# Optimization experiments

Hardware: AMD Instinct MI355X
Metric: run time of the kernel (lower is better)

The kernel has to match this reference:

```python
import jax, jax.numpy as jnp
import numpy as np

N_HEADS = 16
N_KV_HEADS = 4
WINDOW = 128
THETA = 10000.0


def _rope_cos_sin(T, half):
    inv = 1.0 / (THETA ** (jnp.arange(half, dtype=jnp.float32) / half))
    f = jnp.arange(T, dtype=jnp.float32)[:, None] * inv[None, :]  # (T, half)
    return jnp.cos(f), jnp.sin(f)


def _apply_rope(x, cos, sin):
    # x: (B, H, T, hd); interleaved (real, imag) pairs like torch view_as_complex
    xr, xi = x[..., 0::2], x[..., 1::2]
    out_r = xr * cos - xi * sin
    out_i = xr * sin + xi * cos
    return jnp.stack([out_r, out_i], axis=-1).reshape(x.shape)


def setup_inputs() -> dict:
    key = jax.random.key(0)
    ks = jax.random.split(key, 6)
    B, T, C = 1, 4096, 2048
    kvC = (C // N_HEADS) * N_KV_HEADS
    return {
        "x": jax.random.normal(ks[0], (B, T, C), dtype=jnp.float32),
        "wq": jax.random.normal(ks[1], (C, C), dtype=jnp.float32) * 0.02,
        "wk": jax.random.normal(ks[2], (C, kvC), dtype=jnp.float32) * 0.02,
        "wv": jax.random.normal(ks[3], (C, kvC), dtype=jnp.float32) * 0.02,
        "wo": jax.random.normal(ks[4], (C, C), dtype=jnp.float32) * 0.02,
        "sink": jnp.zeros((1, N_HEADS, 1, 1), dtype=jnp.float32),
    }


def reference(x, wq, wk, wv, wo, sink):
    B, T, C = x.shape
    hd = C // N_HEADS
    n_rep = N_HEADS // N_KV_HEADS

    q = (x @ wq).reshape(B, T, N_HEADS, hd).transpose(0, 2, 1, 3)    # (B,H,T,hd)
    k = (x @ wk).reshape(B, T, N_KV_HEADS, hd).transpose(0, 2, 1, 3)  # (B,Hkv,T,hd)
    v = (x @ wv).reshape(B, T, N_KV_HEADS, hd).transpose(0, 2, 1, 3)

    cos, sin = _rope_cos_sin(T, hd // 2)  # (T, hd/2), broadcasts over (B,H,T,hd/2)
    q = _apply_rope(q, cos, sin)
    k = _apply_rope(k, cos, sin)

    # GQA head expansion (repeat_interleave over head dim)
    k = jnp.repeat(k, n_rep, axis=1)
    v = jnp.repeat(v, n_rep, axis=1)

    att = jnp.einsum("bhqd,bhkd->bhqk", q, k) * (hd ** -0.5) + sink

    # symmetric sliding-window band: |i - j| <= window//2
    idx = jnp.arange(T)
    band = jnp.abs(idx[:, None] - idx[None, :]) <= (WINDOW // 2)
    att = jnp.where(band[None, None, :, :], att, -jnp.inf)

    att = jax.nn.softmax(att, axis=-1)
    # torch code replaces NaN rows (fully-masked) with uniform; band always has diag so no-op
    att = jnp.where(jnp.isnan(att), 1.0 / T, att)

    out = jnp.einsum("bhqk,bhkd->bqhd", att, v).reshape(B, T, C)
    return out @ wo
```

## Files before the change

kernel.cpp:

```cpp
#include <hip/hip_runtime.h>
#include <stdint.h>

#define T_SEQ 4096
#define C_DIM 2048
#define HD 128

typedef unsigned short ushort_t;
typedef __attribute__((ext_vector_type(8))) short shortx8;
typedef __attribute__((ext_vector_type(4))) float floatx4;
typedef __attribute__((ext_vector_type(8))) unsigned short u16x8;
typedef __attribute__((ext_vector_type(4))) unsigned short u16x4;

__device__ __forceinline__ ushort_t f2bf(float f) {
  union { float f; uint32_t u; } v; v.f = f;
  v.u += 0x7fffu + ((v.u >> 16) & 1u);
  return (ushort_t)(v.u >> 16);
}
__device__ __forceinline__ void load_lds16(const ushort_t* g, ushort_t* l) {
  __builtin_amdgcn_global_load_lds(
      (const __attribute__((address_space(1))) unsigned int*)g,
      (__attribute__((address_space(3))) unsigned int*)l, 16, 0, 0);
}

__global__ __launch_bounds__(256) void prep_kernel(
    const float* __restrict__ wq, const float* __restrict__ wk,
    const float* __restrict__ wv, const float* __restrict__ wo,
    const float* __restrict__ x,
    ushort_t* __restrict__ BtAll, ushort_t* __restrict__ woT,
    ushort_t* __restrict__ xb) {
  const int bid = blockIdx.x;
  const int tid = threadIdx.x;
  if (bid >= 2560) {
    int i = (bid - 2560) * 256 + tid;
    float4 v = ((const float4*)x)[i];
    u16x4 o; o[0] = f2bf(v.x); o[1] = f2bf(v.y); o[2] = f2bf(v.z); o[3] = f2bf(v.w);
    ((u16x4*)xb)[i] = o;
    return;
  }
  const float* src; ushort_t* dst; int C, bx, by;
  if (bid < 1024) { src = wq; dst = BtAll; C = 2048; bx = bid & 31; by = bid >> 5; }
  else if (bid < 1280) { int b = bid - 1024; src = wk; dst = BtAll + (size_t)2048 * 2048; C = 512; bx = b & 7; by = b >> 3; }
  else if (bid < 1536) { int b = bid - 1280; src = wv; dst = BtAll + (size_t)2560 * 2048; C = 512; bx = b & 7; by = b >> 3; }
  else { int b = bid - 1536; src = wo; dst = woT; C = 2048; bx = b & 31; by = b >> 5; }
  const int R = 2048;

  __shared__ float tile[64][65];
  const int c0 = bx * 64, r0 = by * 64;
  for (int i = tid; i < 1024; i += 256) {
    int r = i >> 4, cc = (i & 15) * 4;
    float4 v = *(const float4*)&src[(size_t)(r0 + r) * C + c0 + cc];
    tile[r][cc] = v.x; tile[r][cc + 1] = v.y; tile[r][cc + 2] = v.z; tile[r][cc + 3] = v.w;
  }
  __syncthreads();
  for (int i = tid; i < 512; i += 256) {
    int oc = i >> 3;
    int g = (i & 7) * 8;
    u16x8 o;
    for (int j = 0; j < 8; ++j) o[j] = f2bf(tile[g + j][oc]);
    *(u16x8*)&dst[(size_t)(c0 + oc) * R + r0 + g] = o;
  }
}

struct GemmAcc { floatx4 a[4][4]; };

__device__ __forceinline__ void gemm_core_bk64(
    const ushort_t* __restrict__ A, const ushort_t* __restrict__ Bt,
    ushort_t* As, ushort_t* Bs, GemmAcc& acc,
    int m0, int n0, int K, int tid, int lane, int wave, int quad, int l16,
    int wm, int wn) {
  const int nk = K >> 6;
  for (int kk = 0; kk < nk; ++kk) {
    const int k0 = kk << 6;
    for (int r = 0; r < 4; ++r) {
      int e = r * 256 + tid;
      int row = e >> 3;
      int p = e & 7;
      int g = (p - row) & 7;
      const ushort_t* ga = A + (size_t)(m0 + row) * K + k0 + g * 8;
      const ushort_t* gb = Bt + (size_t)(n0 + row) * K + k0 + g * 8;
      ushort_t* la = As + (size_t)(r * 256 + (tid & 192)) * 8;
      ushort_t* lb = Bs + (size_t)(r * 256 + (tid & 192)) * 8;
      load_lds16(ga, la);
      load_lds16(gb, lb);
    }
    __syncthreads();
    for (int ks = 0; ks < 2; ++ks) {
      shortx8 af[4], bfr[4];
      for (int i = 0; i < 4; ++i) {
        int ar = wm + i * 16 + l16;
        af[i] = *(const shortx8*)(As + ar * 64 + (((ks << 2) + quad + ar) & 7) * 8);
        int br = wn + i * 16 + l16;
        bfr[i] = *(const shortx8*)(Bs + br * 64 + (((ks << 2) + quad + br) & 7) * 8);
      }
      for (int i = 0; i < 4; ++i)
        for (int j = 0; j < 4; ++j)
          acc.a[i][j] = __builtin_amdgcn_mfma_f32_16x16x32_bf16(af[i], bfr[j], acc.a[i][j], 0, 0, 0);
    }
    __syncthreads();
  }
}

__global__ __launch_bounds__(256, 3) void gemm_qkv(
    const ushort_t* __restrict__ A, const ushort_t* __restrict__ Bt,
    ushort_t* __restrict__ qbb, ushort_t* __restrict__ kbb,
    ushort_t* __restrict__ vtb) {
  __shared__ __align__(16) ushort_t As[128 * 64];
  __shared__ __align__(16) ushort_t Bs[128 * 64];
  const int tid = threadIdx.x;
  const int lane = tid & 63;
  const int wave = tid >> 6;
  const int quad = lane >> 4;
  const int l16 = lane & 15;
  const int m0 = blockIdx.y * 128;
  const int n0 = blockIdx.x * 128;
  const int wm = (wave & 1) * 64;
  const int wn = (wave >> 1) * 64;

  GemmAcc acc = {};
  gemm_core_bk64(A, Bt, As, Bs, acc, m0, n0, 2048, tid, lane, wave, quad, l16, wm, wn);

  if (blockIdx.x < 20) {
    const bool isq = (blockIdx.x < 16);
    const int par = l16 & 1;
    for (int j = 0; j < 4; ++j) {
      int col = n0 + wn + j * 16 + l16;
      int irot = (col & 127) >> 1;
      float inv = __expf(-0.14391157f * (float)irot);
      for (int i = 0; i < 4; ++i) {
        int t0r = m0 + wm + i * 16 + quad * 4;
        for (int r = 0; r < 4; ++r) {
          float val = acc.a[i][j][r];
          float other = __shfl_xor(val, 1, 64);
          float sn, cs;
          __sincosf((float)(t0r + r) * inv, &sn, &cs);
          float outv = par ? (other * sn + val * cs) : (val * cs - other * sn);
          if (isq) qbb[(size_t)(t0r + r) * 2048 + col] = f2bf(outv);
          else     kbb[(size_t)(t0r + r) * 512 + (col - 2048)] = f2bf(outv);
        }
      }
    }
  } else {
    for (int j = 0; j < 4; ++j) {
      int dim = n0 + wn + j * 16 + l16 - 2560;
      for (int i = 0; i < 4; ++i) {
        int t0r = m0 + wm + i * 16 + quad * 4;
        u16x4 o;
        for (int r = 0; r < 4; ++r) o[r] = f2bf(acc.a[i][j][r]);
        *(u16x4*)&vtb[(size_t)dim * T_SEQ + t0r] = o;
      }
    }
  }
}

__global__ __launch_bounds__(256, 3) void gemm_bf16(
    const ushort_t* __restrict__ A, const ushort_t* __restrict__ Bt,
    float* __restrict__ C, int M, int N, int K) {
  __shared__ __align__(16) ushort_t As[128 * 64];
  __shared__ __align__(16) ushort_t Bs[128 * 64];
  const int tid = threadIdx.x;
  const int lane = tid & 63;
  const int wave = tid >> 6;
  const int quad = lane >> 4;
  const int l16 = lane & 15;
  const int m0 = blockIdx.y * 128;
  const int n0 = blockIdx.x * 128;
  const int wm = (wave & 1) * 64;
  const int wn = (wave >> 1) * 64;

  GemmAcc acc = {};
  gemm_core_bk64(A, Bt, As, Bs, acc, m0, n0, K, tid, lane, wave, quad, l16, wm, wn);

  for (int i = 0; i < 4; ++i)
    for (int j = 0; j < 4; ++j) {
      int col = n0 + wn + j * 16 + l16;
      int rbase = m0 + wm + i * 16 + quad * 4;
      for (int r = 0; r < 4; ++r)
        C[(size_t)(rbase + r) * N + col] = acc.a[i][j][r];
    }
}

#define LSTR 168
__global__ __launch_bounds__(256, 2) void attn_kernel(
    const ushort_t* __restrict__ qbb, const ushort_t* __restrict__ kbb,
    const ushort_t* __restrict__ vtb, ushort_t* __restrict__ ao) {
  __shared__ __align__(16) ushort_t QP[64 * LSTR];
  __shared__ __align__(16) ushort_t KV[160 * LSTR];

  const int tid = threadIdx.x;
  const int lane = tid & 63;
  const int wave = tid >> 6;
  const int l16 = lane & 15;
  const int quad = lane >> 4;
  const int h0 = blockIdx.x * 2;
  const int kvh = h0 >> 2;
  const int t0 = blockIdx.y * 32;
  const int kstart = t0 - 64;
  const int hsel = wave & 1;
  const int qh = wave >> 1;
  const float scale = 0.08838834764831845f;

  for (int c = tid; c < 1024; c += 256) {
    int row = c >> 4, c8 = c & 15;
    int h = h0 + (row >> 5);
    int q = t0 + (row & 31);
    u16x8 v = *(const u16x8*)&qbb[(size_t)q * C_DIM + h * HD + c8 * 8];
    *(u16x8*)&QP[row * LSTR + c8 * 8] = v;
  }
  for (int c = tid; c < 2560; c += 256) {
    int row = c >> 4, c8 = c & 15;
    int t = kstart + row;
    u16x8 v;
    if (t >= 0 && t < T_SEQ) {
      v = *(const u16x8*)&kbb[(size_t)t * 512 + kvh * HD + c8 * 8];
    } else {
      for (int z = 0; z < 8; ++z) v[z] = 0;
    }
    *(u16x8*)&KV[row * LSTR + c8 * 8] = v;
  }
  __syncthreads();

  floatx4 acc[10] = {};
  const int arow = hsel * 32 + qh * 16 + l16;
  for (int ks = 0; ks < 4; ++ks) {
    shortx8 af = *(const shortx8*)&QP[arow * LSTR + ks * 32 + quad * 8];
    for (int kt = 0; kt < 10; ++kt) {
      shortx8 bf = *(const shortx8*)&KV[(kt * 16 + l16) * LSTR + ks * 32 + quad * 8];
      acc[kt] = __builtin_amdgcn_mfma_f32_16x16x32_bf16(af, bf, acc[kt], 0, 0, 0);
    }
  }

  float mrow[4] = {-3e38f, -3e38f, -3e38f, -3e38f};
  for (int kt = 0; kt < 10; ++kt) {
    int col = kt * 16 + l16;
    int kg = kstart + col;
    for (int r = 0; r < 4; ++r) {
      int row = qh * 16 + quad * 4 + r;
      bool valid = (kg >= 0) && (kg < T_SEQ) && (col >= row) && (col <= row + 128);
      float s = valid ? acc[kt][r] * scale : -3e38f;
      acc[kt][r] = s;
      mrow[r] = fmaxf(mrow[r], s);
    }
  }
  for (int off = 1; off < 16; off <<= 1)
    for (int r = 0; r < 4; ++r)
      mrow[r] = fmaxf(mrow[r], __shfl_xor(mrow[r], off, 64));
  float rl[4];
  for (int r = 0; r < 4; ++r) {
    float s = 0.f;
    for (int kt = 0; kt < 10; ++kt) {
      float p = expf(acc[kt][r] - mrow[r]);
      acc[kt][r] = p;
      s += p;
    }
    rl[r] = s;
  }
  for (int off = 1; off < 16; off <<= 1)
    for (int r = 0; r < 4; ++r) rl[r] += __shfl_xor(rl[r], off, 64);
  for (int r = 0; r < 4; ++r) rl[r] = 1.0f / rl[r];

  __syncthreads();

  for (int kt = 0; kt < 10; ++kt) {
    int col = kt * 16 + l16;
    for (int r = 0; r < 4; ++r) {
      int row = hsel * 32 + qh * 16 + quad * 4 + r;
      QP[row * LSTR + col] = f2bf(acc[kt][r] * rl[r]);
    }
  }
  for (int c = tid; c < 2560; c += 256) {
    int dim = c / 20, c8 = c % 20;
    int k0 = kstart + c8 * 8;
    const ushort_t* g = &vtb[(size_t)(kvh * HD + dim) * T_SEQ];
    u16x8 v;
    if (k0 >= 0 && k0 + 7 < T_SEQ) {
      v = *(const u16x8*)&g[k0];
    } else {
      for (int z = 0; z < 8; ++z) {
        int kk = k0 + z;
        v[z] = (kk >= 0 && kk < T_SEQ) ? g[kk] : (ushort_t)0;
      }
    }
    *(u16x8*)&KV[dim * LSTR + c8 * 8] = v;
  }
  __syncthreads();

  floatx4 oacc[8] = {};
  const int prow = hsel * 32 + qh * 16 + l16;
  for (int ks = 0; ks < 5; ++ks) {
    shortx8 pf = *(const shortx8*)&QP[prow * LSTR + ks * 32 + quad * 8];
    for (int dt = 0; dt < 8; ++dt) {
      shortx8 vf = *(const shortx8*)&KV[(dt * 16 + l16) * LSTR + ks * 32 + quad * 8];
      oacc[dt] = __builtin_amdgcn_mfma_f32_16x16x32_bf16(pf, vf, oacc[dt], 0, 0, 0);
    }
  }

  const int h = h0 + hsel;
  for (int r = 0; r < 4; ++r) {
    int row = t0 + qh * 16 + quad * 4 + r;
    for (int dt = 0; dt < 8; ++dt) {
      int dim = dt * 16 + l16;
      ao[(size_t)row * C_DIM + h * HD + dim] = f2bf(oacc[dt][r]);
    }
  }
}

extern "C" void kernel_launch(void* const* d_in, const int* in_sizes, int n_in,
                              void* d_out, int out_size, void* d_ws, size_t ws_size,
                              hipStream_t stream) {
  const float* x  = (const float*)d_in[0];
  const float* wq = (const float*)d_in[1];
  const float* wk = (const float*)d_in[2];
  const float* wv = (const float*)d_in[3];
  const float* wo = (const float*)d_in[4];
  float* out = (float*)d_out;

  char* ws = (char*)d_ws;
  ushort_t* BtAll = (ushort_t*)(ws);
  ushort_t* woT   = (ushort_t*)(ws + 12582912);
  ushort_t* xb    = (ushort_t*)(ws + 20971520);
  ushort_t* qbb   = (ushort_t*)(ws + 37748736);
  ushort_t* kbb   = (ushort_t*)(ws + 54525952);
  ushort_t* vtb   = (ushort_t*)(ws + 58720256);
  ushort_t* ao    = (ushort_t*)(ws + 62914560);

  prep_kernel<<<10752, 256, 0, stream>>>(wq, wk, wv, wo, x, BtAll, woT, xb);

  gemm_qkv<<<dim3(24, 32), 256, 0, stream>>>(xb, BtAll, qbb, kbb, vtb);

  attn_kernel<<<dim3(8, 128), 256, 0, stream>>>(qbb, kbb, vtb, ao);

  gemm_bf16<<<dim3(16, 32), 256, 0, stream>>>(ao, woT, out, 4096, 2048, 2048);
}
```

Measured before the change: 243.8 us.

## Replace QKV GEMM with 256x256 double-buffered 8-wave kernel and fast exp

The QKV projection GEMM is rewritten to use 256x256 output tiles with 512 threads. It double-buffers LDS, prefetches global-to-LDS loads interleaved with the MFMA phases, sets wave priority around the MFMAs, and applies a swizzled block order for L2 locality. The larger tiles give more data reuse per loaded byte and hide load latency, at the cost of more LDS and register pressure and only 192 blocks, which may leave the 256 CUs underfilled. Separately, the attention softmax switches from expf to __expf, which is cheaper but less precise.

```diff
diff --git a/kernel.cpp b/kernel.cpp
--- a/kernel.cpp
+++ b/kernel.cpp
@@ -100,58 +100,6 @@
   }
 }
 
-__global__ __launch_bounds__(256, 3) void gemm_qkv(
-    const ushort_t* __restrict__ A, const ushort_t* __restrict__ Bt,
-    ushort_t* __restrict__ qbb, ushort_t* __restrict__ kbb,
-    ushort_t* __restrict__ vtb) {
-  __shared__ __align__(16) ushort_t As[128 * 64];
-  __shared__ __align__(16) ushort_t Bs[128 * 64];
-  const int tid = threadIdx.x;
-  const int lane = tid & 63;
-  const int wave = tid >> 6;
-  const int quad = lane >> 4;
-  const int l16 = lane & 15;
-  const int m0 = blockIdx.y * 128;
-  const int n0 = blockIdx.x * 128;
-  const int wm = (wave & 1) * 64;
-  const int wn = (wave >> 1) * 64;
-
-  GemmAcc acc = {};
-  gemm_core_bk64(A, Bt, As, Bs, acc, m0, n0, 2048, tid, lane, wave, quad, l16, wm, wn);
-
-  if (blockIdx.x < 20) {
-    const bool isq = (blockIdx.x < 16);
-    const int par = l16 & 1;
-    for (int j = 0; j < 4; ++j) {
-      int col = n0 + wn + j * 16 + l16;
-      int irot = (col & 127) >> 1;
-      float inv = __expf(-0.14391157f * (float)irot);
-      for (int i = 0; i < 4; ++i) {
-        int t0r = m0 + wm + i * 16 + quad * 4;
-        for (int r = 0; r < 4; ++r) {
-          float val = acc.a[i][j][r];
-          float other = __shfl_xor(val, 1, 64);
-          float sn, cs;
-          __sincosf((float)(t0r + r) * inv, &sn, &cs);
-          float outv = par ? (other * sn + val * cs) : (val * cs - other * sn);
-          if (isq) qbb[(size_t)(t0r + r) * 2048 + col] = f2bf(outv);
-          else     kbb[(size_t)(t0r + r) * 512 + (col - 2048)] = f2bf(outv);
-        }
-      }
-    }
-  } else {
-    for (int j = 0; j < 4; ++j) {
-      int dim = n0 + wn + j * 16 + l16 - 2560;
-      for (int i = 0; i < 4; ++i) {
-        int t0r = m0 + wm + i * 16 + quad * 4;
-        u16x4 o;
-        for (int r = 0; r < 4; ++r) o[r] = f2bf(acc.a[i][j][r]);
-        *(u16x4*)&vtb[(size_t)dim * T_SEQ + t0r] = o;
-      }
-    }
-  }
-}
-
 __global__ __launch_bounds__(256, 3) void gemm_bf16(
     const ushort_t* __restrict__ A, const ushort_t* __restrict__ Bt,
     float* __restrict__ C, int M, int N, int K) {
@@ -179,6 +127,143 @@
     }
 }
 
+#define BARF() do { __builtin_amdgcn_s_barrier(); asm volatile("" ::: "memory"); } while (0)
+
+__global__ __launch_bounds__(512, 2) void gemm_qkv256(
+    const ushort_t* __restrict__ A, const ushort_t* __restrict__ Bt,
+    ushort_t* __restrict__ qbb, ushort_t* __restrict__ kbb,
+    ushort_t* __restrict__ vtb) {
+  __shared__ __align__(16) ushort_t SA[2][16384];
+  __shared__ __align__(16) ushort_t SB[2][16384];
+  const int tid = threadIdx.x;
+  const int lane = tid & 63;
+  const int w = tid >> 6;
+  const int l16 = lane & 15;
+  const int quad = lane >> 4;
+  const int wm = (w >> 2) * 128;
+  const int wn = (w & 3) * 64;
+  const int aq = wm + (w & 3) * 16;
+  const int bq = wn + (w >> 2) * 16;
+  const int gl8 = lane >> 3;
+  const int gch = ((lane & 7) - gl8) & 7;
+
+  const int bid = blockIdx.x;
+  const int swz = (bid & 7) * 24 + (bid >> 3);
+  const int n0 = (swz % 12) * 256;
+  const int m0 = (swz / 12) * 256;
+
+  const int off0 = l16 * 64 + ((quad + l16) & 7) * 8;
+  const int off1 = l16 * 64 + ((4 + quad + l16) & 7) * 8;
+
+  floatx4 acc[8][4] = {};
+
+  auto issue2 = [&](const ushort_t* __restrict__ G, int gRow, ushort_t* L, int r0, int k0) {
+#pragma unroll
+    for (int u = 0; u < 2; ++u) {
+      const ushort_t* src = G + (size_t)(gRow + r0 + u * 8 + gl8) * 2048 + k0 + gch * 8;
+      load_lds16(src, L + (r0 + u * 8) * 64);
+    }
+  };
+
+  issue2(A, m0, SA[0], aq, 0);        issue2(A, m0, SA[0], aq + 64, 0);
+  issue2(Bt, n0, SB[0], bq, 0);       issue2(Bt, n0, SB[0], bq + 32, 0);
+  issue2(A, m0, SA[1], aq, 64);       issue2(A, m0, SA[1], aq + 64, 64);
+  issue2(Bt, n0, SB[1], bq, 64);      issue2(Bt, n0, SB[1], bq + 32, 64);
+  asm volatile("s_waitcnt vmcnt(8)" ::: "memory");
+  BARF();
+
+  for (int t2 = 0; t2 < 16; ++t2) {
+#pragma unroll
+    for (int half = 0; half < 2; ++half) {
+      const int t = t2 * 2 + half;
+      const ushort_t* SAb = SA[half];
+      const ushort_t* SBb = SB[half];
+      ushort_t* SAo = SA[half ^ 1];
+      ushort_t* SBo = SB[half ^ 1];
+#pragma unroll
+      for (int p = 0; p < 4; ++p) {
+        const int ih = p >> 1, jh = p & 1;
+        shortx8 af0[4], af1[4], bf0[2], bf1[2];
+#pragma unroll
+        for (int i2 = 0; i2 < 4; ++i2) {
+          const int rb = (wm + (ih * 4 + i2) * 16) * 64;
+          af0[i2] = *(const shortx8*)&SAb[rb + off0];
+          af1[i2] = *(const shortx8*)&SAb[rb + off1];
+        }
+#pragma unroll
+        for (int j2 = 0; j2 < 2; ++j2) {
+          const int rb = (wn + (jh * 2 + j2) * 16) * 64;
+          bf0[j2] = *(const shortx8*)&SBb[rb + off0];
+          bf1[j2] = *(const shortx8*)&SBb[rb + off1];
+        }
+        if (p == 0)      { if (t > 0 && t + 1 < 32) issue2(A, m0, SAo, aq + 64, (t + 1) * 64); }
+        else if (p == 1) { if (t > 0 && t + 1 < 32) issue2(Bt, n0, SBo, bq + 32, (t + 1) * 64); }
+        else if (p == 2) { if (t + 2 < 32) issue2(A, m0, (ushort_t*)SAb, aq, (t + 2) * 64); }
+        else             { if (t + 2 < 32) issue2(Bt, n0, (ushort_t*)SBb, bq, (t + 2) * 64); }
+        BARF();
+        asm volatile("s_waitcnt lgkmcnt(0)" ::: "memory");
+        __builtin_amdgcn_s_setprio(1);
+#pragma unroll
+        for (int ks = 0; ks < 2; ++ks)
+#pragma unroll
+          for (int i2 = 0; i2 < 4; ++i2)
+#pragma unroll
+            for (int j2 = 0; j2 < 2; ++j2)
+              acc[ih * 4 + i2][jh * 2 + j2] = __builtin_amdgcn_mfma_f32_16x16x32_bf16(
+                  ks ? af1[i2] : af0[i2], ks ? bf1[j2] : bf0[j2],
+                  acc[ih * 4 + i2][jh * 2 + j2], 0, 0, 0);
+        __builtin_amdgcn_s_setprio(0);
+        if (p == 3) {
+          if (t < 30)       { asm volatile("s_waitcnt vmcnt(4)" ::: "memory"); }
+          else if (t == 30) { asm volatile("s_waitcnt vmcnt(0)" ::: "memory"); }
+        }
+        BARF();
+      }
+    }
+  }
+
+  asm volatile("s_waitcnt vmcnt(0) lgkmcnt(0)" ::: "memory");
+  BARF();
+
+  if (n0 < 2560) {
+    const bool isq = (n0 < 2048);
+    const int par = l16 & 1;
+#pragma unroll
+    for (int j = 0; j < 4; ++j) {
+      int col = n0 + wn + j * 16 + l16;
+      int irot = (col & 127) >> 1;
+      float inv = __expf(-0.14391157f * (float)irot);
+#pragma unroll
+      for (int i = 0; i < 8; ++i) {
+        int t0r = m0 + wm + i * 16 + quad * 4;
+#pragma unroll
+        for (int r = 0; r < 4; ++r) {
+          float val = acc[i][j][r];
+          float other = __shfl_xor(val, 1, 64);
+          float sn, cs;
+          __sincosf((float)(t0r + r) * inv, &sn, &cs);
+          float outv = par ? (other * sn + val * cs) : (val * cs - other * sn);
+          if (isq) qbb[(size_t)(t0r + r) * 2048 + col] = f2bf(outv);
+          else     kbb[(size_t)(t0r + r) * 512 + (col - 2048)] = f2bf(outv);
+        }
+      }
+    }
+  } else {
+#pragma unroll
+    for (int j = 0; j < 4; ++j) {
+      int dim = n0 + wn + j * 16 + l16 - 2560;
+#pragma unroll
+      for (int i = 0; i < 8; ++i) {
+        int t0r = m0 + wm + i * 16 + quad * 4;
+        u16x4 o;
+#pragma unroll
+        for (int r = 0; r < 4; ++r) o[r] = f2bf(acc[i][j][r]);
+        *(u16x4*)&vtb[(size_t)dim * T_SEQ + t0r] = o;
+      }
+    }
+  }
+}
+
 #define LSTR 168
 __global__ __launch_bounds__(256, 2) void attn_kernel(
     const ushort_t* __restrict__ qbb, const ushort_t* __restrict__ kbb,
@@ -248,7 +333,7 @@
   for (int r = 0; r < 4; ++r) {
     float s = 0.f;
     for (int kt = 0; kt < 10; ++kt) {
-      float p = expf(acc[kt][r] - mrow[r]);
+      float p = __expf(acc[kt][r] - mrow[r]);
       acc[kt][r] = p;
       s += p;
     }
@@ -325,7 +410,7 @@
 
   prep_kernel<<<10752, 256, 0, stream>>>(wq, wk, wv, wo, x, BtAll, woT, xb);
 
-  gemm_qkv<<<dim3(24, 32), 256, 0, stream>>>(xb, BtAll, qbb, kbb, vtb);
+  gemm_qkv256<<<192, 512, 0, stream>>>(xb, BtAll, qbb, kbb, vtb);
 
   attn_kernel<<<dim3(8, 128), 256, 0, stream>>>(qbb, kbb, vtb, ao);
 
```

Result: slower. 266.8 us (+9.5%).
